# Performance work log

Hardware: AMD Instinct MI355X
Metric: run time of the kernel (lower is better)

## Reference

```python
import jax, jax.numpy as jnp
import numpy as np

EPS = 1e-5

def _gru(m, h, wih, whh, bih, bhh):
    gi = m @ wih.T + bih
    gh = h @ whh.T + bhh
    ir, iz, inn = jnp.split(gi, 3, axis=-1)
    hr, hz, hn = jnp.split(gh, 3, axis=-1)
    r = jax.nn.sigmoid(ir + hr)
    z = jax.nn.sigmoid(iz + hz)
    n = jnp.tanh(inn + r * hn)
    return (1.0 - z) * n + z * h

def _mggc(h, src, dst, etype, coeff, w, wih, whh, bih, bhh, num_nodes):
    # w: [L, T, C, C]; per-edge-type linear transform, scatter-add aggregation, GRU update
    for l in range(w.shape[0]):
        tr = jnp.einsum('nc,tcd->tnd', h, w[l])            # [T, N, C]
        msg = tr[etype, src] * coeff[src][:, None]          # [E, C] gather by (edge type, source)
        aggr = jax.ops.segment_sum(msg, dst, num_segments=num_nodes)
        h = _gru(aggr, h, wih, whh, bih, bhh)
    return h

def _bn(x, g, b):
    mu = x.mean(axis=0)
    var = x.var(axis=0)
    return (x - mu) * jax.lax.rsqrt(var + EPS) * g + b

def _lstm_cell(inp, h, c, wih, whh, b):
    gates = inp @ wih.T + h @ whh.T + b
    i, f, g, o = jnp.split(gates, 4, axis=-1)
    c = jax.nn.sigmoid(f) * c + jax.nn.sigmoid(i) * jnp.tanh(g)
    h = jax.nn.sigmoid(o) * jnp.tanh(c)
    return h, c

def _set2set(x, batch, num_graphs, wih0, whh0, b0, wih1, whh1, b1, steps=5):
    C = x.shape[1]
    B = num_graphs
    q_star = jnp.zeros((B, 2 * C), x.dtype)
    h0 = jnp.zeros((B, C), x.dtype); c0 = h0; h1 = h0; c1 = h0
    for _ in range(steps):
        h0, c0 = _lstm_cell(q_star, h0, c0, wih0, whh0, b0)
        h1, c1 = _lstm_cell(h0, h1, c1, wih1, whh1, b1)
        q = h1                                              # [B, C]
        e = jnp.sum(x * q[batch], axis=-1)                  # [N]
        emax = jax.ops.segment_max(e, batch, num_segments=B)
        ex = jnp.exp(e - emax[batch])
        denom = jax.ops.segment_sum(ex, batch, num_segments=B)
        a = ex / denom[batch]                               # scatter-softmax over graphs
        r = jax.ops.segment_sum(a[:, None] * x, batch, num_segments=B)
        q_star = jnp.concatenate([q, r], axis=1)
    return q_star                                           # [B, 2C]

def _forward(x, edge_attr, conv_w, conv_wih, conv_whh, conv_bih, conv_bhh, conv_nt,
             s2s1_wih0, s2s1_whh0, s2s1_b0, s2s1_wih1, s2s1_whh1, s2s1_b1,
             s2s2_wih0, s2s2_whh0, s2s2_b0, s2s2_wih1, s2s2_whh1, s2s2_b1,
             bn_g, bn_b, prebn_g, prebn_b,
             fc_w0, fc_b0, fc_w1, fc_b1, fc_w2, fc_b2,
             fcbn_g0, fcbn_b0, fcbn_g1, fcbn_b1,
             edge_index, node_type, batch, assign_src, assign_dst, edge_index_2, batch_2, num_graphs):
    N = x.shape[0]
    N2 = batch_2.shape[0]
    etype = jnp.argmax(edge_attr[:, :4], axis=1)           # edge type from one-hot part of edge_attr
    src, dst = edge_index[0], edge_index[1]
    h = x
    for i in range(3):
        coeff = conv_nt[i][node_type]                      # per-node-type coefficient
        h = _mggc(h, src, dst, etype, coeff, conv_w[i], conv_wih[i], conv_whh[i], conv_bih[i], conv_bhh[i], N)
        h = jax.nn.relu(_bn(h, bn_g[i], bn_b[i]))
    x1 = _set2set(h, batch, num_graphs, s2s1_wih0, s2s1_whh0, s2s1_b0, s2s1_wih1, s2s1_whh1, s2s1_b1)
    # avg_pool: mean of level-1 node features into level-2 clusters
    cnt = jax.ops.segment_sum(jnp.ones((assign_dst.shape[0],), x.dtype), assign_dst, num_segments=N2)
    h2 = jax.ops.segment_sum(h[assign_src], assign_dst, num_segments=N2) / jnp.maximum(cnt, 1.0)[:, None]
    src2, dst2 = edge_index_2[0], edge_index_2[1]
    etype2 = jnp.zeros((src2.shape[0],), jnp.int32)
    ones2 = jnp.ones((N2,), x.dtype)
    h2 = jax.nn.relu(_mggc(h2, src2, dst2, etype2, ones2, conv_w[3], conv_wih[3], conv_whh[3], conv_bih[3], conv_bhh[3], N2))
    h2 = jax.nn.relu(_mggc(h2, src2, dst2, etype2, ones2, conv_w[4], conv_wih[4], conv_whh[4], conv_bih[4], conv_bhh[4], N2))
    x2 = _set2set(h2, batch_2, num_graphs, s2s2_wih0, s2s2_whh0, s2s2_b0, s2s2_wih1, s2s2_whh1, s2s2_b1)
    z = jnp.concatenate([x1, x2], axis=1)                  # [B, 4C] = [B, 256]
    z = _bn(z, prebn_g, prebn_b)
    z = jax.nn.relu(_bn(z @ fc_w0.T + fc_b0, fcbn_g0, fcbn_b0))  # dropout: eval-mode identity
    z = jax.nn.relu(_bn(z @ fc_w1.T + fc_b1, fcbn_g1, fcbn_b1))
    return z @ fc_w2.T + fc_b2                             # [B, 1]

def setup_inputs() -> dict:
    C, L, T, NT = 64, 3, 4, 9
    N, E, N2, E2, A, B = 60000, 600000, 20000, 150000, 60000, 256
    key = jax.random.key(0)
    ks = iter(jax.random.split(key, 48))
    nrm = lambda shape, s: jax.random.normal(next(ks), shape, jnp.float32) * s
    inp = {}
    inp['x'] = nrm((N, C), 1.0)
    inp['edge_attr'] = jax.random.uniform(next(ks), (E, 10), jnp.float32)
    inp['conv_w'] = nrm((5, L, T, C, C), 0.125)
    inp['conv_wih'] = nrm((5, 3 * C, C), 0.125)
    inp['conv_whh'] = nrm((5, 3 * C, C), 0.125)
    inp['conv_bih'] = jnp.zeros((5, 3 * C), jnp.float32)
    inp['conv_bhh'] = jnp.zeros((5, 3 * C), jnp.float32)
    inp['conv_nt'] = 1.0 + nrm((5, NT), 0.1)
    for nm in ('s2s1', 's2s2'):
        inp[nm + '_wih0'] = nrm((4 * C, 2 * C), 0.09)
        inp[nm + '_whh0'] = nrm((4 * C, C), 0.125)
        inp[nm + '_b0'] = jnp.zeros((4 * C,), jnp.float32)
        inp[nm + '_wih1'] = nrm((4 * C, C), 0.125)
        inp[nm + '_whh1'] = nrm((4 * C, C), 0.125)
        inp[nm + '_b1'] = jnp.zeros((4 * C,), jnp.float32)
    inp['bn_g'] = jnp.ones((3, C), jnp.float32)
    inp['bn_b'] = jnp.zeros((3, C), jnp.float32)
    inp['prebn_g'] = jnp.ones((4 * C,), jnp.float32)
    inp['prebn_b'] = jnp.zeros((4 * C,), jnp.float32)
    inp['fc_w0'] = nrm((128, 256), 0.0625)
    inp['fc_b0'] = jnp.zeros((128,), jnp.float32)
    inp['fc_w1'] = nrm((64, 128), 0.09)
    inp['fc_b1'] = jnp.zeros((64,), jnp.float32)
    inp['fc_w2'] = nrm((1, 64), 0.125)
    inp['fc_b2'] = jnp.zeros((1,), jnp.float32)
    inp['fcbn_g0'] = jnp.ones((128,), jnp.float32)
    inp['fcbn_b0'] = jnp.zeros((128,), jnp.float32)
    inp['fcbn_g1'] = jnp.ones((64,), jnp.float32)
    inp['fcbn_b1'] = jnp.zeros((64,), jnp.float32)
    inp['edge_index'] = jax.random.randint(next(ks), (2, E), 0, N)
    inp['node_type'] = jax.random.randint(next(ks), (N,), 0, NT)
    inp['batch'] = jnp.sort(jax.random.randint(next(ks), (N,), 0, B))
    inp['assign_src'] = jax.random.randint(next(ks), (A,), 0, N)
    inp['assign_dst'] = jax.random.randint(next(ks), (A,), 0, N2)
    inp['edge_index_2'] = jax.random.randint(next(ks), (2, E2), 0, N2)
    inp['batch_2'] = jnp.sort(jax.random.randint(next(ks), (N2,), 0, B))
    inp['num_graphs'] = B
    return inp

def reference(x, edge_attr, conv_w, conv_wih, conv_whh, conv_bih, conv_bhh, conv_nt,
              s2s1_wih0, s2s1_whh0, s2s1_b0, s2s1_wih1, s2s1_whh1, s2s1_b1,
              s2s2_wih0, s2s2_whh0, s2s2_b0, s2s2_wih1, s2s2_whh1, s2s2_b1,
              bn_g, bn_b, prebn_g, prebn_b,
              fc_w0, fc_b0, fc_w1, fc_b1, fc_w2, fc_b2,
              fcbn_g0, fcbn_b0, fcbn_g1, fcbn_b1,
              edge_index, node_type, batch, assign_src, assign_dst, edge_index_2, batch_2, num_graphs):
    return _forward(x, edge_attr, conv_w, conv_wih, conv_whh, conv_bih, conv_bhh, conv_nt,
                    s2s1_wih0, s2s1_whh0, s2s1_b0, s2s1_wih1, s2s1_whh1, s2s1_b1,
                    s2s2_wih0, s2s2_whh0, s2s2_b0, s2s2_wih1, s2s2_whh1, s2s2_b1,
                    bn_g, bn_b, prebn_g, prebn_b,
                    fc_w0, fc_b0, fc_w1, fc_b1, fc_w2, fc_b2,
                    fcbn_g0, fcbn_b0, fcbn_g1, fcbn_b1,
                    edge_index, node_type, batch, assign_src, assign_dst, edge_index_2, batch_2, num_graphs)
```

## Files before the change

### kernel.cpp

```cpp
#include <hip/hip_runtime.h>

#define NN1 60000
#define EE1 600000
#define NN2 20000
#define EE2 150000
#define AA  60000

__device__ __forceinline__ float sigf(float x){ return 1.f/(1.f+expf(-x)); }
__device__ __forceinline__ float rlane(float v, int sl){
  return __int_as_float(__builtin_amdgcn_readlane(__float_as_int(v), sl));
}
#define RL4(SL) hx = rlane(ld.x, SL); hy = rlane(ld.y, SL); hz = rlane(ld.z, SL); hw = rlane(ld.w, SL);
#define FMA4(A, W) A = fmaf(hx, W.x, A); A = fmaf(hy, W.y, A); A = fmaf(hz, W.z, A); A = fmaf(hw, W.w, A);

__global__ void k_relu(float* a, int n){
  int i = blockIdx.x*blockDim.x + threadIdx.x;
  if (i < n) a[i] = fmaxf(a[i], 0.f);
}
__global__ void k_copy(const float* __restrict__ a, float* __restrict__ o, int n){
  int i = blockIdx.x*blockDim.x + threadIdx.x;
  if (i < n) o[i] = a[i];
}

__global__ void k_etype(const float* __restrict__ ea, int* __restrict__ etype, int E){
  int e = blockIdx.x*blockDim.x + threadIdx.x;
  if (e >= E) return;
  const float* p = ea + (size_t)e*10;
  float best = p[0]; int bi = 0;
  #pragma unroll
  for (int k = 1; k < 4; ++k){ float v = p[k]; if (v > best){ best = v; bi = k; } }
  etype[e] = bi;
}

__global__ void k_coeff(const float* __restrict__ nt, const int* __restrict__ node_type,
                        float* __restrict__ coeff, int N){
  int n = blockIdx.x*blockDim.x + threadIdx.x;
  if (n < N) coeff[n] = nt[node_type[n]];
}

__global__ void k_batchptr(const int* __restrict__ batch, int* __restrict__ rb, int N, int B){
  int n = blockIdx.x*blockDim.x + threadIdx.x;
  if (n >= N) return;
  int b = batch[n];
  if (n == 0){ for (int g = 0; g <= b; ++g) rb[g] = 0; }
  else {
    int pb = batch[n-1];
    for (int g = pb+1; g <= b; ++g) rb[g] = n;
  }
  if (n == N-1){ for (int g = b+1; g <= B; ++g) rb[g] = N; }
}

__global__ void k_prep_msgw(const float* __restrict__ w, float* __restrict__ w4){
  int idx = blockIdx.x*256 + threadIdx.x;
  if (idx >= 245760) return;
  int m = idx >> 12, r = idx & 4095;
  int c4 = r >> 8, d = (r >> 2) & 63, q = r & 3;
  w4[idx] = w[m*4096 + (4*c4+q)*64 + d];
}
__global__ void k_prep_gruw(const float* __restrict__ wih, const float* __restrict__ whh,
                            float* __restrict__ wihT, float* __restrict__ wihW,
                            float* __restrict__ whh4){
  int idx = blockIdx.x*256 + threadIdx.x;
  if (idx >= 61440) return;
  {
    int l = idx / 12288, r = idx % 12288;
    int t = r >> 12, rr = r & 4095;
    int c4 = rr >> 8, d = (rr >> 2) & 63, q = rr & 3;
    wihT[idx] = wih[l*12288 + (64*t + d)*64 + 4*c4 + q];
  }
  {
    int l = idx / 12288, rr = idx % 12288;
    int e = rr >> 2, q = rr & 3;
    int c4 = e / 192, j = e - c4*192;
    wihW[idx] = wih[l*12288 + j*64 + 4*c4 + q];
    whh4[idx] = whh[l*12288 + j*64 + 4*c4 + q];
  }
}

__global__ void k_s2strans(const float* __restrict__ wih0, const float* __restrict__ whh0,
                           const float* __restrict__ wih1, const float* __restrict__ whh1,
                           float* __restrict__ T){
  int idx = blockIdx.x*256 + threadIdx.x;
  if (idx < 32768){ int k = idx >> 8, j = idx & 255; T[idx] = wih0[j*128 + k]; }
  else if (idx < 49152){ int r = idx - 32768; int k = r >> 8, j = r & 255; T[idx] = whh0[j*64 + k]; }
  else if (idx < 65536){ int r = idx - 49152; int k = r >> 8, j = r & 255; T[idx] = wih1[j*64 + k]; }
  else if (idx < 81920){ int r = idx - 65536; int k = r >> 8, j = r & 255; T[idx] = whh1[j*64 + k]; }
}

__global__ void k_hist(const int* __restrict__ dst, int* __restrict__ cnt, int E){
  int e = blockIdx.x*blockDim.x + threadIdx.x;
  if (e >= E) return;
  atomicAdd(&cnt[dst[e]], 1);
}
__global__ void k_chunksum(const int* __restrict__ cnt, int* __restrict__ csum, int M){
  __shared__ int sh[256];
  int base = blockIdx.x*1024;
  int s = 0;
  for (int i = threadIdx.x; i < 1024; i += 256){
    int idx = base + i;
    if (idx < M) s += cnt[idx];
  }
  sh[threadIdx.x] = s;
  __syncthreads();
  for (int o = 128; o; o >>= 1){
    if (threadIdx.x < o) sh[threadIdx.x] += sh[threadIdx.x + o];
    __syncthreads();
  }
  if (threadIdx.x == 0) csum[blockIdx.x] = sh[0];
}
__global__ void k_chunkscan(int* __restrict__ csum, int nchunk){
  __shared__ int sh[256];
  int i = threadIdx.x;
  int v = (i < nchunk) ? csum[i] : 0;
  sh[i] = v; __syncthreads();
  for (int o = 1; o < 256; o <<= 1){
    int y = (i >= o) ? sh[i-o] : 0;
    __syncthreads();
    sh[i] += y;
    __syncthreads();
  }
  if (i < nchunk) csum[i] = sh[i] - v;
  if (i == 255) csum[nchunk] = sh[255];
}
__global__ void k_chunkapply(const int* __restrict__ cnt, const int* __restrict__ csum,
                             int* __restrict__ R, int* __restrict__ cur, int M){
  __shared__ int sh[256];
  int base = blockIdx.x*1024;
  int i0 = base + threadIdx.x*4;
  int v[4]; int s = 0;
  #pragma unroll
  for (int k = 0; k < 4; ++k){ int idx = i0 + k; v[k] = (idx < M) ? cnt[idx] : 0; s += v[k]; }
  sh[threadIdx.x] = s; __syncthreads();
  for (int o = 1; o < 256; o <<= 1){
    int y = (threadIdx.x >= o) ? sh[threadIdx.x-o] : 0;
    __syncthreads();
    sh[threadIdx.x] += y;
    __syncthreads();
  }
  int run = csum[blockIdx.x] + sh[threadIdx.x] - s;
  #pragma unroll
  for (int k = 0; k < 4; ++k){
    int idx = i0 + k;
    if (idx < M){ R[idx] = run; cur[idx] = run; run += v[k]; }
  }
  if (threadIdx.x == 255 && base + 1024 >= M) R[M] = csum[blockIdx.x] + sh[255];
}
__global__ void k_scatter(const int* __restrict__ src, const int* __restrict__ dst,
                          const int* __restrict__ etype, int* __restrict__ cur,
                          int* __restrict__ ep, int E, int N){
  int e = blockIdx.x*blockDim.x + threadIdx.x;
  if (e >= E) return;
  int t = etype ? etype[e] : 0;
  int pos = atomicAdd(&cur[dst[e]], 1);
  ep[pos] = t*N + src[e];
}


__global__ __launch_bounds__(1024, 4) void k_tr4d(
    const float* __restrict__ h, const float* __restrict__ W4,
    const float* __restrict__ coeff, float* __restrict__ tr, int N){
  extern __shared__ float4 wl[];
  for (int i = threadIdx.x; i < 4096; i += 1024) wl[i] = ((const float4*)W4)[i];
  __syncthreads();
  int lane = threadIdx.x & 63, wv = threadIdx.x >> 6;
  int ng = N >> 2, stride = gridDim.x*16;
  for (int g = blockIdx.x*16 + wv; g < ng; g += stride){
    int n0 = g << 2;
    float4 ld = ((const float4*)(h + ((size_t)n0 << 6)))[lane];
    float a00=0.f,a01=0.f,a02=0.f,a03=0.f;
    float a10=0.f,a11=0.f,a12=0.f,a13=0.f;
    float a20=0.f,a21=0.f,a22=0.f,a23=0.f;
    float a30=0.f,a31=0.f,a32=0.f,a33=0.f;
    for (int c4 = 0; c4 < 16; ++c4){
      int wb = (c4 << 6) + lane;
      float4 w0 = wl[wb], w1 = wl[1024+wb], w2 = wl[2048+wb], w3 = wl[3072+wb];
      float hx, hy, hz, hw;
      RL4(c4)     FMA4(a00,w0) FMA4(a10,w1) FMA4(a20,w2) FMA4(a30,w3)
      RL4(16|c4)  FMA4(a01,w0) FMA4(a11,w1) FMA4(a21,w2) FMA4(a31,w3)
      RL4(32|c4)  FMA4(a02,w0) FMA4(a12,w1) FMA4(a22,w2) FMA4(a32,w3)
      RL4(48|c4)  FMA4(a03,w0) FMA4(a13,w1) FMA4(a23,w2) FMA4(a33,w3)
    }
    float4 cv = ((const float4*)coeff)[g];
    a00*=cv.x; a01*=cv.y; a02*=cv.z; a03*=cv.w;
    a10*=cv.x; a11*=cv.y; a12*=cv.z; a13*=cv.w;
    a20*=cv.x; a21*=cv.y; a22*=cv.z; a23*=cv.w;
    a30*=cv.x; a31*=cv.y; a32*=cv.z; a33*=cv.w;
    float* o0 = tr + ((size_t)n0 << 6) + lane;
    o0[0]=a00; o0[64]=a01; o0[128]=a02; o0[192]=a03;
    float* o1 = tr + (((size_t)N + n0) << 6) + lane;
    o1[0]=a10; o1[64]=a11; o1[128]=a12; o1[192]=a13;
    float* o2 = tr + (((size_t)2*N + n0) << 6) + lane;
    o2[0]=a20; o2[64]=a21; o2[128]=a22; o2[192]=a23;
    float* o3 = tr + (((size_t)3*N + n0) << 6) + lane;
    o3[0]=a30; o3[64]=a31; o3[128]=a32; o3[192]=a33;
  }
}

__global__ __launch_bounds__(256) void k_tr1(
    const float* __restrict__ h, const float* __restrict__ W4,
    const float* __restrict__ coeff, float* __restrict__ tr, int N){
  __shared__ float4 wl[1024];
  for (int i = threadIdx.x; i < 1024; i += 256) wl[i] = ((const float4*)W4)[i];
  __syncthreads();
  int lane = threadIdx.x & 63, w = threadIdx.x >> 6;
  int ng = N >> 2, stride = gridDim.x*4;
  for (int g = blockIdx.x*4 + w; g < ng; g += stride){
    int n0 = g << 2;
    float4 ld = ((const float4*)(h + ((size_t)n0 << 6)))[lane];
    float a0=0.f, a1=0.f, a2=0.f, a3=0.f;
    for (int c4 = 0; c4 < 16; ++c4){
      float4 w0 = wl[(c4 << 6) + lane];
      float hx, hy, hz, hw;
      RL4(c4)       FMA4(a0, w0)
      RL4(16|c4)    FMA4(a1, w0)
      RL4(32|c4)    FMA4(a2, w0)
      RL4(48|c4)    FMA4(a3, w0)
    }
    if (coeff){
      float4 cv = ((const float4*)coeff)[g];
      a0 *= cv.x; a1 *= cv.y; a2 *= cv.z; a3 *= cv.w;
    }
    float* o0 = tr + ((size_t)n0 << 6) + lane;
    o0[0] = a0; o0[64] = a1; o0[128] = a2; o0[192] = a3;
  }
}

__global__ void k_sweep_p(const float* __restrict__ tr, const int* __restrict__ R,
                          const int* __restrict__ ep, float* __restrict__ aggr, int N){
  int w = threadIdx.x >> 6, lane = threadIdx.x & 63;
  int d = blockIdx.x*4 + w;
  if (d >= N) return;
  int p = R[d], pend = R[d+1];
  float a0=0.f, a1=0.f, a2=0.f, a3=0.f;
  while (p < pend){
    int m = pend - p; if (m > 64) m = 64;
    int ev = (lane < m) ? ep[p + lane] : 0;
    int j = 0;
    for (; j + 4 <= m; j += 4){
      int r0 = __shfl(ev, j),   r1 = __shfl(ev, j+1);
      int r2 = __shfl(ev, j+2), r3 = __shfl(ev, j+3);
      float v0 = tr[((size_t)r0 << 6) + lane];
      float v1 = tr[((size_t)r1 << 6) + lane];
      float v2 = tr[((size_t)r2 << 6) + lane];
      float v3 = tr[((size_t)r3 << 6) + lane];
      a0 += v0; a1 += v1; a2 += v2; a3 += v3;
    }
    for (; j < m; ++j){
      int r0 = __shfl(ev, j);
      a0 += tr[((size_t)r0 << 6) + lane];
    }
    p += m;
  }
  aggr[(size_t)d*64 + lane] = (a0 + a1) + (a2 + a3);
}

__global__ __launch_bounds__(256) void k_tr3(
    const float* __restrict__ h, const float* __restrict__ W4,
    float* __restrict__ tr, int N){
  __shared__ float4 wl[3072];
  for (int i = threadIdx.x; i < 3072; i += 256) wl[i] = ((const float4*)W4)[i];
  __syncthreads();
  int lane = threadIdx.x & 63, w = threadIdx.x >> 6;
  int ng = N >> 2, stride = gridDim.x*4;
  for (int g = blockIdx.x*4 + w; g < ng; g += stride){
    int n0 = g << 2;
    float4 ld = ((const float4*)(h + ((size_t)n0 << 6)))[lane];
    float a00=0.f,a01=0.f,a02=0.f,a03=0.f;
    float a10=0.f,a11=0.f,a12=0.f,a13=0.f;
    float a20=0.f,a21=0.f,a22=0.f,a23=0.f;
    for (int c4 = 0; c4 < 16; ++c4){
      float4 w0 = wl[(c4 << 6) + lane];
      float4 w1 = wl[1024 + (c4 << 6) + lane];
      float4 w2 = wl[2048 + (c4 << 6) + lane];
      float hx, hy, hz, hw;
      RL4(c4)       FMA4(a00, w0) FMA4(a10, w1) FMA4(a20, w2)
      RL4(16|c4)    FMA4(a01, w0) FMA4(a11, w1) FMA4(a21, w2)
      RL4(32|c4)    FMA4(a02, w0) FMA4(a12, w1) FMA4(a22, w2)
      RL4(48|c4)    FMA4(a03, w0) FMA4(a13, w1) FMA4(a23, w2)
    }
    float* o0 = tr + ((size_t)n0 << 6) + lane;
    o0[0] = a00; o0[64] = a01; o0[128] = a02; o0[192] = a03;
    float* o1 = tr + (((size_t)N + n0) << 6) + lane;
    o1[0] = a10; o1[64] = a11; o1[128] = a12; o1[192] = a13;
    float* o2 = tr + (((size_t)2*N + n0) << 6) + lane;
    o2[0] = a20; o2[64] = a21; o2[128] = a22; o2[192] = a23;
  }
}

#define GACC2(K, R, Z, P, Q) { \
  float4 av = stg[((K) << 4) + c4]; \
  float4 hv = stg[64 + ((K) << 4) + c4]; \
  R = fmaf(av.x,iwr.x,R); R = fmaf(av.y,iwr.y,R); R = fmaf(av.z,iwr.z,R); R = fmaf(av.w,iwr.w,R); \
  R = fmaf(hv.x,hwr.x,R); R = fmaf(hv.y,hwr.y,R); R = fmaf(hv.z,hwr.z,R); R = fmaf(hv.w,hwr.w,R); \
  Z = fmaf(av.x,iwz.x,Z); Z = fmaf(av.y,iwz.y,Z); Z = fmaf(av.z,iwz.z,Z); Z = fmaf(av.w,iwz.w,Z); \
  Z = fmaf(hv.x,hwz.x,Z); Z = fmaf(hv.y,hwz.y,Z); Z = fmaf(hv.z,hwz.z,Z); Z = fmaf(hv.w,hwz.w,Z); \
  P = fmaf(av.x,iwn.x,P); P = fmaf(av.y,iwn.y,P); P = fmaf(av.z,iwn.z,P); P = fmaf(av.w,iwn.w,P); \
  Q = fmaf(hv.x,hwn.x,Q); Q = fmaf(hv.y,hwn.y,Q); Q = fmaf(hv.z,hwn.z,Q); Q = fmaf(hv.w,hwn.w,Q); }
#define GFIN(K, R, Z, P, Q) { \
    size_t off = base + ((size_t)(K) << 6) + lane; \
    float hv = h[off]; \
    float r = sigf(R), z = sigf(Z); \
    float nn = tanhf(P + r*Q); \
    h[off] = (1.f - z)*nn + z*hv; }
__global__ __launch_bounds__(1024, 4) void k_gru_fused(
    const float* __restrict__ aggr, float* __restrict__ h,
    const float* __restrict__ wihW, const float* __restrict__ whhW,
    const float* __restrict__ bih, const float* __restrict__ bhh, int N){
  extern __shared__ float4 wl[];
  for (int i = threadIdx.x; i < 6144; i += 1024)
    wl[i] = (i < 3072) ? ((const float4*)wihW)[i] : ((const float4*)whhW)[i - 3072];
  __syncthreads();
  const float4* wi = wl;
  const float4* wh = wl + 3072;
  int lane = threadIdx.x & 63, wv = threadIdx.x >> 6;
  float4* stg = wl + 6144 + wv*128;
  float br  = bih[lane]     + bhh[lane];
  float bz  = bih[64+lane]  + bhh[64+lane];
  float bp  = bih[128+lane];
  float bq  = bhh[128+lane];
  int ng = N >> 2, stride = gridDim.x*16;
  for (int g = blockIdx.x*16 + wv; g < ng; g += stride){
    int n0 = g << 2;
    size_t base = (size_t)n0 << 6;
    float4 la = ((const float4*)(aggr + base))[lane];
    float4 ld = ((const float4*)(h + base))[lane];
    stg[lane] = la;
    stg[64 + lane] = ld;
    float r0=br, r1=br, r2=br, r3=br;
    float z0=bz, z1=bz, z2=bz, z3=bz;
    float p0=bp, p1=bp, p2=bp, p3=bp;
    float q0=bq, q1=bq, q2=bq, q3=bq;
    for (int c4 = 0; c4 < 16; ++c4){
      int wb = c4*192 + lane;
      float4 iwr = wi[wb], iwz = wi[wb+64], iwn = wi[wb+128];
      float4 hwr = wh[wb], hwz = wh[wb+64], hwn = wh[wb+128];
      GACC2(0, r0, z0, p0, q0)
      GACC2(1, r1, z1, p1, q1)
      GACC2(2, r2, z2, p2, q2)
      GACC2(3, r3, z3, p3, q3)
    }
    GFIN(0, r0, z0, p0, q0)
    GFIN(1, r1, z1, p1, q1)
    GFIN(2, r2, z2, p2, q2)
    GFIN(3, r3, z3, p3, q3)
  }
}

#define GRUACC(SL, RK, ZK, NK) RL4(SL) FMA4(RK, wr) FMA4(ZK, wz) FMA4(NK, wn)
#define GRUFIN(K, RK, ZK, NK) { \
    size_t off = base + (K << 6) + lane; \
    float gir = gi[off], giz = gi[S + off], gin = gi[2*S + off]; \
    float hv = h[off]; \
    float r = sigf(gir + bir + RK); \
    float z = sigf(giz + biz + ZK); \
    float nv = tanhf(gin + bin_ + r*NK); \
    h[off] = (1.f - z)*nv + z*hv; }
__global__ __launch_bounds__(256, 3) void k_gru_finW(
    const float* __restrict__ gi, float* __restrict__ h,
    const float* __restrict__ whh4,
    const float* __restrict__ bih, const float* __restrict__ bhh, int N){
  __shared__ float4 wh[3072];
  for (int i = threadIdx.x; i < 3072; i += 256) wh[i] = ((const float4*)whh4)[i];
  __syncthreads();
  int lane = threadIdx.x & 63, w = threadIdx.x >> 6;
  float bir = bih[lane], biz = bih[64+lane], bin_ = bih[128+lane];
  float bhr = bhh[lane], bhz = bhh[64+lane], bhn = bhh[128+lane];
  size_t S = (size_t)N << 6;
  int ng = N >> 2, stride = gridDim.x*4;
  for (int g = blockIdx.x*4 + w; g < ng; g += stride){
    int n0 = g << 2;
    size_t base = (size_t)n0 << 6;
    float4 ld = ((const float4*)(h + base))[lane];
    float ar0=bhr, ar1=bhr, ar2=bhr, ar3=bhr;
    float az0=bhz, az1=bhz, az2=bhz, az3=bhz;
    float an0=bhn, an1=bhn, an2=bhn, an3=bhn;
    for (int c4 = 0; c4 < 16; ++c4){
      int wb = c4*192 + lane;
      float4 wr = wh[wb];
      float4 wz = wh[wb + 64];
      float4 wn = wh[wb + 128];
      float hx, hy, hz, hw;
      GRUACC(c4,    ar0, az0, an0)
      GRUACC(16|c4, ar1, az1, an1)
      GRUACC(32|c4, ar2, az2, an2)
      GRUACC(48|c4, ar3, az3, an3)
    }
    GRUFIN(0, ar0, az0, an0)
    GRUFIN(1, ar1, az1, an1)
    GRUFIN(2, ar2, az2, an2)
    GRUFIN(3, ar3, az3, an3)
  }
}

__global__ void k_bnstats(const float* __restrict__ h, float* __restrict__ stats, int N){
  int c = threadIdx.x & 63;
  int g = threadIdx.x >> 6;
  float s = 0.f, s2 = 0.f;
  for (int n = blockIdx.x*4 + g; n < N; n += gridDim.x*4){
    float v = h[(size_t)n*64 + c]; s += v; s2 += v*v;
  }
  __shared__ float sh[4][64], sh2[4][64];
  sh[g][c] = s; sh2[g][c] = s2;
  __syncthreads();
  if (g == 0){
    float ts = sh[0][c]+sh[1][c]+sh[2][c]+sh[3][c];
    float t2 = sh2[0][c]+sh2[1][c]+sh2[2][c]+sh2[3][c];
    atomicAdd(&stats[c], ts); atomicAdd(&stats[64+c], t2);
  }
}
__global__ void k_bnapply(float* __restrict__ h, const float* __restrict__ stats,
                          const float* __restrict__ g, const float* __restrict__ b,
                          int N, int relu){
  int i = blockIdx.x*blockDim.x + threadIdx.x;
  if (i >= N*64) return;
  int c = i & 63;
  float inv = 1.f/(float)N;
  float mean = stats[c]*inv;
  float var  = stats[64+c]*inv - mean*mean;
  float y = (h[i]-mean)*rsqrtf(var + 1e-5f)*g[c] + b[c];
  if (relu) y = fmaxf(y, 0.f);
  h[i] = y;
}

__global__ void k_pool_acc(const float* __restrict__ h, const int* __restrict__ asrc,
                           const int* __restrict__ adst, float* __restrict__ h2,
                           float* __restrict__ cnt, int A){
  int i = blockIdx.x*blockDim.x + threadIdx.x;
  if (i >= A*64) return;
  int a = i >> 6, c = i & 63;
  int s = asrc[a], d = adst[a];
  atomicAdd(&h2[(size_t)d*64 + c], h[(size_t)s*64 + c]);
  if (c == 0) atomicAdd(&cnt[d], 1.f);
}
__global__ void k_pool_div(float* __restrict__ h2, const float* __restrict__ cnt, int N){
  int i = blockIdx.x*blockDim.x + threadIdx.x;
  if (i >= N*64) return;
  h2[i] = h2[i] / fmaxf(cnt[i >> 6], 1.f);
}

__global__ __launch_bounds__(1024) void k_set2set(const float* __restrict__ x, const int* __restrict__ rb,
                          const float* __restrict__ T,
                          const float* __restrict__ b0, const float* __restrict__ b1,
                          float* __restrict__ xout){
  int b = blockIdx.x, j = threadIdx.x;
  int w = j >> 6, lane = j & 63;
  __shared__ float qstar[128], h0[64], c0[64], h1[64], c1[64];
  __shared__ float gs[256], wmax[16], wsum[16], racc[16][64];
  if (j < 128) qstar[j] = 0.f;
  if (j < 64){ h0[j] = 0.f; c0[j] = 0.f; h1[j] = 0.f; c1[j] = 0.f; }
  __syncthreads();
  int n0 = rb[b], n1 = rb[b+1];
  const float* T0 = T;
  const float* T1 = T + 32768;
  const float* T2 = T + 49152;
  const float* T3 = T + 65536;
  for (int s = 0; s < 5; ++s){
    if (j < 256){
      float a0 = b0[j], a1 = 0.f, a2 = 0.f, a3 = 0.f;
      #pragma unroll 4
      for (int k = 0; k < 128; k += 4){
        a0 = fmaf(T0[(k+0)*256 + j], qstar[k+0], a0);
        a1 = fmaf(T0[(k+1)*256 + j], qstar[k+1], a1);
        a2 = fmaf(T0[(k+2)*256 + j], qstar[k+2], a2);
        a3 = fmaf(T0[(k+3)*256 + j], qstar[k+3], a3);
      }
      #pragma unroll 4
      for (int k = 0; k < 64; k += 4){
        a0 = fmaf(T1[(k+0)*256 + j], h0[k+0], a0);
        a1 = fmaf(T1[(k+1)*256 + j], h0[k+1], a1);
        a2 = fmaf(T1[(k+2)*256 + j], h0[k+2], a2);
        a3 = fmaf(T1[(k+3)*256 + j], h0[k+3], a3);
      }
      gs[j] = (a0 + a1) + (a2 + a3);
    }
    __syncthreads();
    if (j < 64){
      float ig = sigf(gs[j]);
      float fg = sigf(gs[64+j]);
      float gg = tanhf(gs[128+j]);
      float og = sigf(gs[192+j]);
      float cn = fg*c0[j] + ig*gg;
      c0[j] = cn;
      h0[j] = og*tanhf(cn);
    }
    __syncthreads();
    if (j < 256){
      float a0 = b1[j], a1 = 0.f, a2 = 0.f, a3 = 0.f;
      #pragma unroll 4
      for (int k = 0; k < 64; k += 4){
        a0 = fmaf(T2[(k+0)*256 + j], h0[k+0], a0);
        a1 = fmaf(T2[(k+1)*256 + j], h0[k+1], a1);
        a2 = fmaf(T2[(k+2)*256 + j], h0[k+2], a2);
        a3 = fmaf(T2[(k+3)*256 + j], h0[k+3], a3);
      }
      #pragma unroll 4
      for (int k = 0; k < 64; k += 4){
        a0 = fmaf(T3[(k+0)*256 + j], h1[k+0], a0);
        a1 = fmaf(T3[(k+1)*256 + j], h1[k+1], a1);
        a2 = fmaf(T3[(k+2)*256 + j], h1[k+2], a2);
        a3 = fmaf(T3[(k+3)*256 + j], h1[k+3], a3);
      }
      gs[j] = (a0 + a1) + (a2 + a3);
    }
    __syncthreads();
    if (j < 64){
      float ig = sigf(gs[j]);
      float fg = sigf(gs[64+j]);
      float gg = tanhf(gs[128+j]);
      float og = sigf(gs[192+j]);
      float cn = fg*c1[j] + ig*gg;
      c1[j] = cn;
      float hn = og*tanhf(cn);
      h1[j] = hn;
      qstar[j] = hn;
    }
    __syncthreads();
    float lmax = -3.4e38f, lsum = 0.f, lr = 0.f;
    for (int n = n0 + w; n < n1; n += 16){
      float xv = x[(size_t)n*64 + lane];
      float v = xv*qstar[lane];
      #pragma unroll
      for (int o = 32; o; o >>= 1) v += __shfl_xor(v, o);
      float nm = fmaxf(lmax, v);
      float corr = expf(lmax - nm);
      float e = expf(v - nm);
      lsum = fmaf(lsum, corr, e);
      lr   = fmaf(lr, corr, e*xv);
      lmax = nm;
    }
    if (lane == 0){ wmax[w] = lmax; wsum[w] = lsum; }
    racc[w][lane] = lr;
    __syncthreads();
    if (j < 64){
      float M = wmax[0];
      #pragma unroll
      for (int k = 1; k < 16; ++k) M = fmaxf(M, wmax[k]);
      float denom = 0.f, r = 0.f;
      #pragma unroll
      for (int k = 0; k < 16; ++k){
        float sc = expf(wmax[k] - M);
        denom = fmaf(wsum[k], sc, denom);
        r     = fmaf(racc[k][j], sc, r);
      }
      qstar[64 + j] = (denom > 0.f) ? (r/denom) : 0.f;
    }
    __syncthreads();
  }
  if (j < 128) xout[(size_t)b*128 + j] = qstar[j];
}

__global__ void k_concat(const float* __restrict__ x1, const float* __restrict__ x2,
                         float* __restrict__ z){
  int i = blockIdx.x*blockDim.x + threadIdx.x;
  if (i >= 256*256) return;
  int b = i >> 8, c = i & 255;
  z[i] = (c < 128) ? x1[b*128 + c] : x2[b*128 + (c - 128)];
}
__global__ void k_bn_par(float* __restrict__ X, const float* __restrict__ g,
                         const float* __restrict__ b, int F, int relu){
  int f = blockIdx.x, i = threadIdx.x;
  float v = X[(size_t)i*F + f];
  __shared__ float s1[256], s2[256];
  s1[i] = v; s2[i] = v*v;
  __syncthreads();
  for (int o = 128; o; o >>= 1){
    if (i < o){ s1[i] += s1[i+o]; s2[i] += s2[i+o]; }
    __syncthreads();
  }
  float mean = s1[0]*(1.f/256.f);
  float var  = s2[0]*(1.f/256.f) - mean*mean;
  float y = (v - mean)*rsqrtf(var + 1e-5f)*g[f] + b[f];
  if (relu) y = fmaxf(y, 0.f);
  X[(size_t)i*F + f] = y;
}
__global__ void k_fc(const float* __restrict__ X, const float* __restrict__ W,
                     const float* __restrict__ bias, float* __restrict__ Y, int K, int F){
  int b = blockIdx.x, f = threadIdx.x;
  if (f >= F) return;
  const float* xr = X + (size_t)b*K;
  const float* wr = W + (size_t)f*K;
  float acc = bias[f];
  for (int k = 0; k < K; ++k) acc = fmaf(xr[k], wr[k], acc);
  Y[(size_t)b*F + f] = acc;
}
__global__ void k_fc_out(const float* __restrict__ z2, const float* __restrict__ w,
                         const float* __restrict__ bias, float* __restrict__ out){
  int b = blockIdx.x*blockDim.x + threadIdx.x;
  if (b >= 256) return;
  float acc = bias[0];
  #pragma unroll
  for (int k = 0; k < 64; ++k) acc = fmaf(z2[b*64 + k], w[k], acc);
  out[b] = acc;
}

extern "C" void kernel_launch(void* const* d_in, const int* in_sizes, int n_in,
                              void* d_out, int out_size, void* d_ws, size_t ws_size,
                              hipStream_t stream) {
  const float* x_in     = (const float*)d_in[0];
  const float* edge_attr= (const float*)d_in[1];
  const float* conv_w   = (const float*)d_in[2];
  const float* conv_wih = (const float*)d_in[3];
  const float* conv_whh = (const float*)d_in[4];
  const float* conv_bih = (const float*)d_in[5];
  const float* conv_bhh = (const float*)d_in[6];
  const float* conv_nt  = (const float*)d_in[7];
  const float* s1_wih0 = (const float*)d_in[8];
  const float* s1_whh0 = (const float*)d_in[9];
  const float* s1_b0   = (const float*)d_in[10];
  const float* s1_wih1 = (const float*)d_in[11];
  const float* s1_whh1 = (const float*)d_in[12];
  const float* s1_b1   = (const float*)d_in[13];
  const float* s2_wih0 = (const float*)d_in[14];
  const float* s2_whh0 = (const float*)d_in[15];
  const float* s2_b0   = (const float*)d_in[16];
  const float* s2_wih1 = (const float*)d_in[17];
  const float* s2_whh1 = (const float*)d_in[18];
  const float* s2_b1   = (const float*)d_in[19];
  const float* bn_g    = (const float*)d_in[20];
  const float* bn_b    = (const float*)d_in[21];
  const float* prebn_g = (const float*)d_in[22];
  const float* prebn_b = (const float*)d_in[23];
  const float* fc_w0   = (const float*)d_in[24];
  const float* fc_b0   = (const float*)d_in[25];
  const float* fc_w1   = (const float*)d_in[26];
  const float* fc_b1   = (const float*)d_in[27];
  const float* fc_w2   = (const float*)d_in[28];
  const float* fc_b2   = (const float*)d_in[29];
  const float* fcbn_g0 = (const float*)d_in[30];
  const float* fcbn_b0 = (const float*)d_in[31];
  const float* fcbn_g1 = (const float*)d_in[32];
  const float* fcbn_b1 = (const float*)d_in[33];
  const int* edge_index   = (const int*)d_in[34];
  const int* node_type    = (const int*)d_in[35];
  const int* batch        = (const int*)d_in[36];
  const int* assign_src   = (const int*)d_in[37];
  const int* assign_dst   = (const int*)d_in[38];
  const int* edge_index_2 = (const int*)d_in[39];
  const int* batch_2      = (const int*)d_in[40];
  (void)in_sizes; (void)n_in; (void)out_size; (void)ws_size;

  int fused_ok = (hipFuncSetAttribute((const void*)k_gru_fused,
                    hipFuncAttributeMaxDynamicSharedMemorySize, 131072) == hipSuccess);
  int tr4_ok = (hipFuncSetAttribute((const void*)k_tr4d,
                    hipFuncAttributeMaxDynamicSharedMemorySize, 65536) == hipSuccess);

  float* Wp = (float*)d_ws;
  size_t o = 0;
  auto alloc = [&](size_t n){ float* p = Wp + o; o += n; return p; };
  float* h     = alloc((size_t)NN1*64);
  float* tr    = alloc((size_t)4*NN1*64);
  float* aggr  = alloc((size_t)NN1*64);
  float* coeff = alloc(NN1);
  float* h2    = alloc((size_t)NN2*64);
  float* cnt   = alloc(NN2);
  float* x1    = alloc(256*128);
  float* x2    = alloc(256*128);
  float* z     = alloc(256*256);
  float* z1    = alloc(256*128);
  float* z2    = alloc(256*64);
  float* stats = alloc(128);
  float* w4    = alloc(245760);
  float* wihT  = alloc(61440);
  float* wihW  = alloc(61440);
  float* whh4  = alloc(61440);
  float* s2sT1 = alloc(81920);
  float* s2sT2 = alloc(81920);
  int* etype = (int*)alloc(EE1);
  int* cnt1  = (int*)alloc(NN1);
  int* R1    = (int*)alloc(NN1 + 1);
  int* ep1   = (int*)alloc(EE1);
  int* cnt2  = (int*)alloc(NN2);
  int* R2    = (int*)alloc(NN2 + 1);
  int* ep2   = (int*)alloc(EE2);
  int* csum  = (int*)alloc(260);
  int* rb1   = (int*)alloc(257);
  int* rb2   = (int*)alloc(257);

  const int* src1 = edge_index;
  const int* dst1 = edge_index + EE1;
  const int* src2 = edge_index_2;
  const int* dst2 = edge_index_2 + EE2;

  k_etype<<<(EE1+255)/256, 256, 0, stream>>>(edge_attr, etype, EE1);
  k_copy<<<(NN1*64+255)/256, 256, 0, stream>>>(x_in, h, NN1*64);
  k_prep_msgw<<<(245760+255)/256, 256, 0, stream>>>(conv_w, w4);
  k_prep_gruw<<<(61440+255)/256, 256, 0, stream>>>(conv_wih, conv_whh, wihT, wihW, whh4);
  k_s2strans<<<(81920+255)/256, 256, 0, stream>>>(s1_wih0, s1_whh0, s1_wih1, s1_whh1, s2sT1);
  k_s2strans<<<(81920+255)/256, 256, 0, stream>>>(s2_wih0, s2_whh0, s2_wih1, s2_whh1, s2sT2);
  k_batchptr<<<(NN1+255)/256, 256, 0, stream>>>(batch, rb1, NN1, 256);
  k_batchptr<<<(NN2+255)/256, 256, 0, stream>>>(batch_2, rb2, NN2, 256);

  {
    int M = NN1, nchunk = (M + 1023)/1024;
    hipMemsetAsync(cnt1, 0, (size_t)M*sizeof(int), stream);
    k_hist<<<(EE1+255)/256, 256, 0, stream>>>(dst1, cnt1, EE1);
    k_chunksum<<<nchunk, 256, 0, stream>>>(cnt1, csum, M);
    k_chunkscan<<<1, 256, 0, stream>>>(csum, nchunk);
    k_chunkapply<<<nchunk, 256, 0, stream>>>(cnt1, csum, R1, cnt1, M);
    k_scatter<<<(EE1+255)/256, 256, 0, stream>>>(src1, dst1, etype, cnt1, ep1, EE1, NN1);
  }
  {
    int M = NN2, nchunk = (M + 1023)/1024;
    hipMemsetAsync(cnt2, 0, (size_t)M*sizeof(int), stream);
    k_hist<<<(EE2+255)/256, 256, 0, stream>>>(dst2, cnt2, EE2);
    k_chunksum<<<nchunk, 256, 0, stream>>>(cnt2, csum, M);
    k_chunkscan<<<1, 256, 0, stream>>>(csum, nchunk);
    k_chunkapply<<<nchunk, 256, 0, stream>>>(cnt2, csum, R2, cnt2, M);
    k_scatter<<<(EE2+255)/256, 256, 0, stream>>>(src2, dst2, nullptr, cnt2, ep2, EE2, NN2);
  }

  auto gru = [&](float* hbuf, int N, int lidx){
    if (fused_ok){
      k_gru_fused<<<256, 1024, 131072, stream>>>(aggr, hbuf,
          wihW + (size_t)lidx*12288, whh4 + (size_t)lidx*12288,
          conv_bih + lidx*192, conv_bhh + lidx*192, N);
    } else {
      k_tr3<<<768, 256, 0, stream>>>(aggr, wihT + (size_t)lidx*12288, tr, N);
      k_gru_finW<<<768, 256, 0, stream>>>(tr, hbuf, whh4 + (size_t)lidx*12288,
          conv_bih + lidx*192, conv_bhh + lidx*192, N);
    }
  };

  for (int i = 0; i < 3; ++i){
    k_coeff<<<(NN1+255)/256, 256, 0, stream>>>(conv_nt + i*9, node_type, coeff, NN1);
    for (int l = 0; l < 3; ++l){
      const float* W4l = w4 + (size_t)(i*3+l)*16384;
      if (tr4_ok){
        k_tr4d<<<512, 1024, 65536, stream>>>(h, W4l, coeff, tr, NN1);
      } else {
        for (int t = 0; t < 4; ++t)
          k_tr1<<<1024, 256, 0, stream>>>(h, W4l + (size_t)t*4096, coeff,
                                          tr + (size_t)t*NN1*64, NN1);
      }
      k_sweep_p<<<(NN1+3)/4, 256, 0, stream>>>(tr, R1, ep1, aggr, NN1);
      gru(h, NN1, i);
    }
    hipMemsetAsync(stats, 0, 128*sizeof(float), stream);
    k_bnstats<<<256, 256, 0, stream>>>(h, stats, NN1);
    k_bnapply<<<(NN1*64+255)/256, 256, 0, stream>>>(h, stats, bn_g + i*64, bn_b + i*64, NN1, 1);
  }

  k_set2set<<<256, 1024, 0, stream>>>(h, rb1, s2sT1, s1_b0, s1_b1, x1);

  hipMemsetAsync(h2, 0, (size_t)NN2*64*sizeof(float), stream);
  hipMemsetAsync(cnt, 0, (size_t)NN2*sizeof(float), stream);
  k_pool_acc<<<(AA*64+255)/256, 256, 0, stream>>>(h, assign_src, assign_dst, h2, cnt, AA);
  k_pool_div<<<(NN2*64+255)/256, 256, 0, stream>>>(h2, cnt, NN2);

  for (int L = 3; L < 5; ++L){
    for (int l = 0; l < 3; ++l){
      const float* W4l = w4 + (size_t)(L*3+l)*16384;
      k_tr1<<<1250, 256, 0, stream>>>(h2, W4l, nullptr, tr, NN2);
      k_sweep_p<<<(NN2+3)/4, 256, 0, stream>>>(tr, R2, ep2, aggr, NN2);
      gru(h2, NN2, L);
    }
    k_relu<<<(NN2*64+255)/256, 256, 0, stream>>>(h2, NN2*64);
  }

  k_set2set<<<256, 1024, 0, stream>>>(h2, rb2, s2sT2, s2_b0, s2_b1, x2);

  k_concat<<<256, 256, 0, stream>>>(x1, x2, z);
  k_bn_par<<<256, 256, 0, stream>>>(z, prebn_g, prebn_b, 256, 0);
  k_fc<<<256, 128, 0, stream>>>(z, fc_w0, fc_b0, z1, 256, 128);
  k_bn_par<<<128, 256, 0, stream>>>(z1, fcbn_g0, fcbn_b0, 128, 1);
  k_fc<<<256, 64, 0, stream>>>(z1, fc_w1, fc_b1, z2, 128, 64);
  k_bn_par<<<64, 256, 0, stream>>>(z2, fcbn_g1, fcbn_b1, 64, 1);
  k_fc_out<<<4, 64, 0, stream>>>(z2, fc_w2, fc_b2, (float*)d_out);
}
```

Before: 2.035 ms.

## Prefetch next node-group loads in tr/GRU kernels and split set2set LSTM matvec

In the transform kernels (k_tr4d, k_tr1) and the fused GRU kernel, the next iteration's h/aggr rows are loaded ahead of the current iteration's FMA loop, a software-pipelining step meant to hide global load latency. In set2set, the LSTM gate matvecs now use all 1024 threads by splitting the reduction dimension into four parts with partial sums in shared memory, instead of leaving 768 threads idle. The prefetch adds register pressure in kernels already at high occupancy bounds. The split adds a shared-memory reduction and bias add in the gate step.

```diff
diff --git a/kernel.cpp b/kernel.cpp
--- a/kernel.cpp
+++ b/kernel.cpp
@@ -164,9 +164,14 @@
   __syncthreads();
   int lane = threadIdx.x & 63, wv = threadIdx.x >> 6;
   int ng = N >> 2, stride = gridDim.x*16;
-  for (int g = blockIdx.x*16 + wv; g < ng; g += stride){
+  int g0 = blockIdx.x*16 + wv;
+  float4 ld;
+  if (g0 < ng) ld = ((const float4*)(h + ((size_t)(g0 << 2) << 6)))[lane];
+  for (int g = g0; g < ng; g += stride){
     int n0 = g << 2;
-    float4 ld = ((const float4*)(h + ((size_t)n0 << 6)))[lane];
+    int gn = g + stride;
+    float4 ldn = ld;
+    if (gn < ng) ldn = ((const float4*)(h + ((size_t)(gn << 2) << 6)))[lane];
     float a00=0.f,a01=0.f,a02=0.f,a03=0.f;
     float a10=0.f,a11=0.f,a12=0.f,a13=0.f;
     float a20=0.f,a21=0.f,a22=0.f,a23=0.f;
@@ -193,6 +198,7 @@
     o2[0]=a20; o2[64]=a21; o2[128]=a22; o2[192]=a23;
     float* o3 = tr + (((size_t)3*N + n0) << 6) + lane;
     o3[0]=a30; o3[64]=a31; o3[128]=a32; o3[192]=a33;
+    ld = ldn;
   }
 }
 
@@ -204,9 +210,14 @@
   __syncthreads();
   int lane = threadIdx.x & 63, w = threadIdx.x >> 6;
   int ng = N >> 2, stride = gridDim.x*4;
-  for (int g = blockIdx.x*4 + w; g < ng; g += stride){
+  int g0 = blockIdx.x*4 + w;
+  float4 ld;
+  if (g0 < ng) ld = ((const float4*)(h + ((size_t)(g0 << 2) << 6)))[lane];
+  for (int g = g0; g < ng; g += stride){
     int n0 = g << 2;
-    float4 ld = ((const float4*)(h + ((size_t)n0 << 6)))[lane];
+    int gn = g + stride;
+    float4 ldn = ld;
+    if (gn < ng) ldn = ((const float4*)(h + ((size_t)(gn << 2) << 6)))[lane];
     float a0=0.f, a1=0.f, a2=0.f, a3=0.f;
     for (int c4 = 0; c4 < 16; ++c4){
       float4 w0 = wl[(c4 << 6) + lane];
@@ -222,6 +233,7 @@
     }
     float* o0 = tr + ((size_t)n0 << 6) + lane;
     o0[0] = a0; o0[64] = a1; o0[128] = a2; o0[192] = a3;
+    ld = ldn;
   }
 }
 
@@ -319,13 +331,25 @@
   float bp  = bih[128+lane];
   float bq  = bhh[128+lane];
   int ng = N >> 2, stride = gridDim.x*16;
-  for (int g = blockIdx.x*16 + wv; g < ng; g += stride){
+  int g0 = blockIdx.x*16 + wv;
+  float4 la, ld;
+  if (g0 < ng){
+    size_t b0_ = (size_t)(g0 << 2) << 6;
+    la = ((const float4*)(aggr + b0_))[lane];
+    ld = ((const float4*)(h + b0_))[lane];
+  }
+  for (int g = g0; g < ng; g += stride){
     int n0 = g << 2;
     size_t base = (size_t)n0 << 6;
-    float4 la = ((const float4*)(aggr + base))[lane];
-    float4 ld = ((const float4*)(h + base))[lane];
     stg[lane] = la;
     stg[64 + lane] = ld;
+    int gn = g + stride;
+    float4 la2 = la, ld2 = ld;
+    if (gn < ng){
+      size_t bn = (size_t)(gn << 2) << 6;
+      la2 = ((const float4*)(aggr + bn))[lane];
+      ld2 = ((const float4*)(h + bn))[lane];
+    }
     float r0=br, r1=br, r2=br, r3=br;
     float z0=bz, z1=bz, z2=bz, z3=bz;
     float p0=bp, p1=bp, p2=bp, p3=bp;
@@ -343,6 +367,7 @@
     GFIN(1, r1, z1, p1, q1)
     GFIN(2, r2, z2, p2, q2)
     GFIN(3, r3, z3, p3, q3)
+    la = la2; ld = ld2;
   }
 }
 
@@ -444,8 +469,9 @@
                           float* __restrict__ xout){
   int b = blockIdx.x, j = threadIdx.x;
   int w = j >> 6, lane = j & 63;
+  int part = j >> 8, row = j & 255;
   __shared__ float qstar[128], h0[64], c0[64], h1[64], c1[64];
-  __shared__ float gs[256], wmax[16], wsum[16], racc[16][64];
+  __shared__ float gp[4][256], wmax[16], wsum[16], racc[16][64];
   if (j < 128) qstar[j] = 0.f;
   if (j < 64){ h0[j] = 0.f; c0[j] = 0.f; h1[j] = 0.f; c1[j] = 0.f; }
   __syncthreads();
@@ -455,60 +481,67 @@
   const float* T2 = T + 49152;
   const float* T3 = T + 65536;
   for (int s = 0; s < 5; ++s){
-    if (j < 256){
-      float a0 = b0[j], a1 = 0.f, a2 = 0.f, a3 = 0.f;
-      #pragma unroll 4
-      for (int k = 0; k < 128; k += 4){
-        a0 = fmaf(T0[(k+0)*256 + j], qstar[k+0], a0);
-        a1 = fmaf(T0[(k+1)*256 + j], qstar[k+1], a1);
-        a2 = fmaf(T0[(k+2)*256 + j], qstar[k+2], a2);
-        a3 = fmaf(T0[(k+3)*256 + j], qstar[k+3], a3);
+    {
+      float a0 = 0.f, a1 = 0.f, a2 = 0.f, a3 = 0.f;
+      int kq = part << 5;
+      for (int k = kq; k < kq + 32; k += 4){
+        a0 = fmaf(T0[(k+0)*256 + row], qstar[k+0], a0);
+        a1 = fmaf(T0[(k+1)*256 + row], qstar[k+1], a1);
+        a2 = fmaf(T0[(k+2)*256 + row], qstar[k+2], a2);
+        a3 = fmaf(T0[(k+3)*256 + row], qstar[k+3], a3);
       }
-      #pragma unroll 4
-      for (int k = 0; k < 64; k += 4){
-        a0 = fmaf(T1[(k+0)*256 + j], h0[k+0], a0);
-        a1 = fmaf(T1[(k+1)*256 + j], h0[k+1], a1);
-        a2 = fmaf(T1[(k+2)*256 + j], h0[k+2], a2);
-        a3 = fmaf(T1[(k+3)*256 + j], h0[k+3], a3);
+      int kh = part << 4;
+      for (int k = kh; k < kh + 16; k += 4){
+        a0 = fmaf(T1[(k+0)*256 + row], h0[k+0], a0);
+        a1 = fmaf(T1[(k+1)*256 + row], h0[k+1], a1);
+        a2 = fmaf(T1[(k+2)*256 + row], h0[k+2], a2);
+        a3 = fmaf(T1[(k+3)*256 + row], h0[k+3], a3);
       }
-      gs[j] = (a0 + a1) + (a2 + a3);
+      gp[part][row] = (a0 + a1) + (a2 + a3);
     }
     __syncthreads();
     if (j < 64){
-      float ig = sigf(gs[j]);
-      float fg = sigf(gs[64+j]);
-      float gg = tanhf(gs[128+j]);
-      float og = sigf(gs[192+j]);
-      float cn = fg*c0[j] + ig*gg;
+      float gi_ = b0[j]     + gp[0][j]     + gp[1][j]     + gp[2][j]     + gp[3][j];
+      float gf  = b0[64+j]  + gp[0][64+j]  + gp[1][64+j]  + gp[2][64+j]  + gp[3][64+j];
+      float gg  = b0[128+j] + gp[0][128+j] + gp[1][128+j] + gp[2][128+j] + gp[3][128+j];
+      float go  = b0[192+j] + gp[0][192+j] + gp[1][192+j] + gp[2][192+j] + gp[3][192+j];
+      float ig = sigf(gi_);
+      float fg = sigf(gf);
+      float ggt = tanhf(gg);
+      float og = sigf(go);
+      float cn = fg*c0[j] + ig*ggt;
       c0[j] = cn;
       h0[j] = og*tanhf(cn);
     }
     __syncthreads();
-    if (j < 256){
-      float a0 = b1[j], a1 = 0.f, a2 = 0.f, a3 = 0.f;
-      #pragma unroll 4
-      for (int k = 0; k < 64; k += 4){
-        a0 = fmaf(T2[(k+0)*256 + j], h0[k+0], a0);
-        a1 = fmaf(T2[(k+1)*256 + j], h0[k+1], a1);
-        a2 = fmaf(T2[(k+2)*256 + j], h0[k+2], a2);
-        a3 = fmaf(T2[(k+3)*256 + j], h0[k+3], a3);
+    {
+      float a0 = 0.f, a1 = 0.f, a2 = 0.f, a3 = 0.f;
+      int kh = part << 4;
+      for (int k = kh; k < kh + 16; k += 4){
+        a0 = fmaf(T2[(k+0)*256 + row], h0[k+0], a0);
+        a1 = fmaf(T2[(k+1)*256 + row], h0[k+1], a1);
+        a2 = fmaf(T2[(k+2)*256 + row], h0[k+2], a2);
+        a3 = fmaf(T2[(k+3)*256 + row], h0[k+3], a3);
       }
-      #pragma unroll 4
-      for (int k = 0; k < 64; k += 4){
-        a0 = fmaf(T3[(k+0)*256 + j], h1[k+0], a0);
-        a1 = fmaf(T3[(k+1)*256 + j], h1[k+1], a1);
-        a2 = fmaf(T3[(k+2)*256 + j], h1[k+2], a2);
-        a3 = fmaf(T3[(k+3)*256 + j], h1[k+3], a3);
+      for (int k = kh; k < kh + 16; k += 4){
+        a0 = fmaf(T3[(k+0)*256 + row], h1[k+0], a0);
+        a1 = fmaf(T3[(k+1)*256 + row], h1[k+1], a1);
+        a2 = fmaf(T3[(k+2)*256 + row], h1[k+2], a2);
+        a3 = fmaf(T3[(k+3)*256 + row], h1[k+3], a3);
       }
-      gs[j] = (a0 + a1) + (a2 + a3);
+      gp[part][row] = (a0 + a1) + (a2 + a3);
     }
     __syncthreads();
     if (j < 64){
-      float ig = sigf(gs[j]);
-      float fg = sigf(gs[64+j]);
-      float gg = tanhf(gs[128+j]);
-      float og = sigf(gs[192+j]);
-      float cn = fg*c1[j] + ig*gg;
+      float gi_ = b1[j]     + gp[0][j]     + gp[1][j]     + gp[2][j]     + gp[3][j];
+      float gf  = b1[64+j]  + gp[0][64+j]  + gp[1][64+j]  + gp[2][64+j]  + gp[3][64+j];
+      float gg  = b1[128+j] + gp[0][128+j] + gp[1][128+j] + gp[2][128+j] + gp[3][128+j];
+      float go  = b1[192+j] + gp[0][192+j] + gp[1][192+j] + gp[2][192+j] + gp[3][192+j];
+      float ig = sigf(gi_);
+      float fg = sigf(gf);
+      float ggt = tanhf(gg);
+      float og = sigf(go);
+      float cn = fg*c1[j] + ig*ggt;
       c1[j] = cn;
       float hn = og*tanhf(cn);
       h1[j] = hn;
```

Result: no change. 2.032 ms (-0.1%).
